# Optimization experiments

Hardware: AMD Instinct MI355X
Metric: run time of the kernel (lower is better)

Reference implementation:

```python
import jax, jax.numpy as jnp
import numpy as np

B, T, D, H, L = 16, 1500, 512, 1024, 20


def setup_inputs() -> dict:
    key = jax.random.key(0)
    ks = jax.random.split(key, 5)
    return {
        "x": jax.random.normal(ks[0], (B, T, D), dtype=jnp.float32),
        "w1": jax.random.normal(ks[1], (D, H), dtype=jnp.float32) * (1.0 / np.sqrt(D)),
        "b1": jax.random.normal(ks[2], (H,), dtype=jnp.float32) * 0.01,
        "wp": jax.random.normal(ks[3], (H, D), dtype=jnp.float32) * (1.0 / np.sqrt(H)),
        "wa": jax.random.normal(ks[4], (D, L), dtype=jnp.float32) * (1.0 / np.sqrt(D)),
    }


def reference(x, w1, b1, wp, wa):
    # x: [B,T,D]
    f1 = jax.nn.relu(x @ w1 + b1)          # [B,T,H]
    p1 = f1 @ wp                            # [B,T,D] (output_dim == input_dim)
    lorder = wa.shape[1]
    t = p1.shape[1]
    # left-pad time axis with lorder-1 zeros so shift i looks at p1[t-i]
    padded = jnp.pad(p1, ((0, 0), (lorder - 1, 0), (0, 0)))  # [B,T+L-1,D]
    # z[..., i] = p1 shifted back by i frames (zero for t-i < 0)
    z = jnp.stack(
        [jax.lax.dynamic_slice_in_dim(padded, lorder - 1 - i, t, axis=1)
         for i in range(lorder)],
        axis=-1,
    )  # [B,T,D,L]
    att = jax.nn.softmax(x @ wa, axis=-1)   # [B,T,L]
    out1 = jnp.einsum('btdl,btl->btd', z, att)
    return x + out1
```

## Files before the change

### kernel.cpp

```cpp
#include <hip/hip_runtime.h>
#include <hip/hip_bf16.h>

#define Bd 16
#define Td 1500
#define Dd 512
#define Hd 1024
#define Ld 20
#define Md (Bd*Td)

using f32x4  = __attribute__((ext_vector_type(4))) float;
using short8 = __attribute__((ext_vector_type(8))) short;

__device__ __forceinline__ unsigned short f2bf(float f) {
    union { float f; unsigned u; } v; v.f = f;
    unsigned r = v.u + 0x7fffu + ((v.u >> 16) & 1u);
    return (unsigned short)(r >> 16);
}
__device__ __forceinline__ float bf2f(unsigned short u) {
    union { unsigned u; float f; } v; v.u = ((unsigned)u) << 16;
    return v.f;
}
__device__ __forceinline__ void gload_lds16(const void* g, void* l) {
    __builtin_amdgcn_global_load_lds(
        (const __attribute__((address_space(1))) unsigned*)g,
        (__attribute__((address_space(3))) unsigned*)l, 16, 0, 0);
}

__device__ __forceinline__ void transpose_body(
    const float* __restrict__ W, unsigned short* __restrict__ WT,
    int K, int N, int n0, int k0, int tid, float (*tile)[33])
{
    const int tx = tid & 31, ty = tid >> 5;
#pragma unroll
    for (int j = 0; j < 32; j += 8)
        tile[ty + j][tx] = W[(size_t)(k0 + ty + j) * N + n0 + tx];
    __syncthreads();
#pragma unroll
    for (int j = 0; j < 32; j += 8)
        WT[(size_t)(n0 + ty + j) * K + k0 + tx] = f2bf(tile[tx][ty + j]);
}

__global__ __launch_bounds__(256) void prep_kernel(
    const float* __restrict__ x,  const float* __restrict__ w1,
    const float* __restrict__ wp, const float* __restrict__ wa,
    unsigned short* __restrict__ xb,  unsigned short* __restrict__ w1T,
    unsigned short* __restrict__ wpT, unsigned short* __restrict__ waT)
{
    __shared__ float tile[32][33];
    const int b = blockIdx.x, tid = threadIdx.x;
    if (b < 6000) {
        size_t i = ((size_t)b * 256 + tid) * 8;
        float4 v0 = *(const float4*)(x + i);
        float4 v1 = *(const float4*)(x + i + 4);
        union { unsigned short us[8]; int4 v; } p;
        p.us[0] = f2bf(v0.x); p.us[1] = f2bf(v0.y); p.us[2] = f2bf(v0.z); p.us[3] = f2bf(v0.w);
        p.us[4] = f2bf(v1.x); p.us[5] = f2bf(v1.y); p.us[6] = f2bf(v1.z); p.us[7] = f2bf(v1.w);
        *(int4*)(xb + i) = p.v;
    } else if (b < 6512) {
        const int idx = b - 6000;
        transpose_body(w1, w1T, Dd, Hd, (idx & 31) * 32, (idx >> 5) * 32, tid, tile);
    } else if (b < 7024) {
        const int idx = b - 6512;
        transpose_body(wp, wpT, Hd, Dd, (idx & 15) * 32, (idx >> 4) * 32, tid, tile);
    } else {
        const int i = (b - 7024) * 256 + tid;
        const int c = i >> 9, d = i & 511;
        waT[i] = (c < Ld) ? f2bf(wa[(size_t)d * Ld + c]) : (unsigned short)0;
    }
}

template<bool RELU_BIAS>
__global__ __launch_bounds__(512) void gemm_lds(
    const unsigned short* __restrict__ A, const unsigned short* __restrict__ BT,
    const float* __restrict__ bias, unsigned short* __restrict__ C,
    int Mdim, int Ndim, int Kdim)
{
    __shared__ __align__(16) unsigned short SH[3 * 8192 + 3 * 4096];

    const int tid  = threadIdx.x;
    const int lane = tid & 63;
    const int wave = tid >> 6;
    const int wr   = wave >> 1, wc = wave & 1;

    const int nx  = gridDim.x;
    const int nwg = nx * gridDim.y;
    const int id  = blockIdx.y * nx + blockIdx.x;
    const int nid = (id & 7) * (nwg >> 3) + (id >> 3);
    const int m0  = (nid / nx) * 256;
    const int n0  = (nid % nx) * 128;

    const int srow  = tid >> 2;
    const int sslot = (tid & 3) ^ ((srow >> 1) & 3);
    int aR0 = m0 + srow;       if (aR0 >= Mdim) aR0 = Mdim - 1;
    int aR1 = m0 + 128 + srow; if (aR1 >= Mdim) aR1 = Mdim - 1;
    const unsigned short* a0p = A  + (size_t)aR0 * Kdim + sslot * 8;
    const unsigned short* a1p = A  + (size_t)aR1 * Kdim + sslot * 8;
    const unsigned short* b0p = BT + (size_t)(n0 + srow) * Kdim + sslot * 8;

    const int rsel = lane & 15;
    const int koff = ((lane >> 4) ^ ((lane >> 1) & 3)) * 8;

    f32x4 acc[4][4] = {};
    const int NT = Kdim >> 5;

    auto stage = [&](int t, int b) {
        const int kk = t * 32;
        gload_lds16(a0p + kk, SH + b * 8192 + wave * 512);
        gload_lds16(a1p + kk, SH + b * 8192 + 4096 + wave * 512);
        gload_lds16(b0p + kk, SH + 24576 + b * 4096 + wave * 512);
    };

    stage(0, 0);
    stage(1, 1);

    int buf = 0;
    for (int t = 0; t < NT; ++t) {
        if (t + 1 < NT) asm volatile("s_waitcnt vmcnt(3)" ::: "memory");
        else            asm volatile("s_waitcnt vmcnt(0)" ::: "memory");
        __builtin_amdgcn_s_barrier();
        asm volatile("" ::: "memory");

        if (t + 2 < NT) {
            int nb = buf + 2; if (nb >= 3) nb -= 3;
            stage(t + 2, nb);
        }

        const unsigned short* as = SH + buf * 8192;
        const unsigned short* bs = SH + 24576 + buf * 4096;
        short8 af[4], bfr[4];
#pragma unroll
        for (int m = 0; m < 4; ++m)
            af[m] = *(const short8*)&as[(wr * 64 + m * 16 + rsel) * 32 + koff];
#pragma unroll
        for (int n = 0; n < 4; ++n)
            bfr[n] = *(const short8*)&bs[(wc * 64 + n * 16 + rsel) * 32 + koff];

        __builtin_amdgcn_s_setprio(1);
#pragma unroll
        for (int m = 0; m < 4; ++m)
#pragma unroll
            for (int n = 0; n < 4; ++n)
                acc[m][n] = __builtin_amdgcn_mfma_f32_16x16x32_bf16(af[m], bfr[n], acc[m][n], 0, 0, 0);
        __builtin_amdgcn_s_setprio(0);

        ++buf; if (buf == 3) buf = 0;
    }

    __syncthreads();
    unsigned short* Cs = SH;

    const int rB = wr * 64 + ((lane >> 4) << 2);
    const int cB = wc * 64;
#pragma unroll
    for (int n = 0; n < 4; ++n) {
        const int col = cB + n * 16 + rsel;
        float bvs = 0.f;
        if (RELU_BIAS) bvs = bias[n0 + col];
        const int s = col >> 3, e = col & 7;
#pragma unroll
        for (int m = 0; m < 4; ++m) {
#pragma unroll
            for (int j = 0; j < 4; ++j) {
                const int r = rB + m * 16 + j;
                float v = acc[m][n][j];
                if (RELU_BIAS) v = fmaxf(v + bvs, 0.f);
                Cs[r * 128 + ((s ^ (r & 7)) << 3) + e] = f2bf(v);
            }
        }
    }
    __syncthreads();

    const int row = tid >> 1;
    const int c0  = (tid & 1) * 64;
    const int gr  = m0 + row;
    if (gr < Mdim) {
#pragma unroll
        for (int i = 0; i < 8; ++i) {
            const int s = (c0 >> 3) + i;
            int4 v = *(const int4*)&Cs[row * 128 + ((s ^ (row & 7)) << 3)];
            *(int4*)&C[(size_t)gr * Ndim + n0 + c0 + i * 8] = v;
        }
    }
}

__global__ __launch_bounds__(256) void att_mfma_kernel(
    const unsigned short* __restrict__ xb, const unsigned short* __restrict__ waT,
    float* __restrict__ att)
{
    __shared__ __align__(16) unsigned short waTs[16 * 1024];
    __shared__ __align__(16) unsigned short As[3][64 * 32];
    __shared__ float sS[64][21];

    const int tid  = threadIdx.x;
    const int lane = tid & 63;
    const int wave = tid >> 6;
    const int m0   = blockIdx.x * 64;

    for (int i = tid; i < 2048; i += 256) {
        const int off = i * 8;
        const int kt = off >> 10, c = (off >> 5) & 31, sl = (off >> 3) & 3;
        const int ssl = sl ^ ((c >> 1) & 3);
        *(short8*)&waTs[off] = *(const short8*)&waT[(size_t)c * Dd + kt * 32 + ssl * 8];
    }
    __syncthreads();

    const int srow  = tid >> 2;
    const int sslot = (tid & 3) ^ ((tid >> 3) & 3);
    const unsigned short* a0p = xb + (size_t)(m0 + srow) * Dd + sslot * 8;

    const int rsel = lane & 15;
    const int koff = ((lane >> 4) ^ ((lane >> 1) & 3)) * 8;

    f32x4 acc[2] = {};

    gload_lds16(a0p, &As[0][wave * 512]);
    gload_lds16(a0p + 32, &As[1][wave * 512]);

    int buf = 0;
    for (int t = 0; t < 16; ++t) {
        if (t < 15) asm volatile("s_waitcnt vmcnt(1)" ::: "memory");
        else        asm volatile("s_waitcnt vmcnt(0)" ::: "memory");
        __builtin_amdgcn_s_barrier();
        asm volatile("" ::: "memory");

        if (t + 2 < 16) {
            int nb = buf + 2; if (nb >= 3) nb -= 3;
            gload_lds16(a0p + (t + 2) * 32, &As[nb][wave * 512]);
        }

        short8 af = *(const short8*)&As[buf][(wave * 16 + rsel) * 32 + koff];
        short8 b0 = *(const short8*)&waTs[t * 1024 + (rsel) * 32 + koff];
        short8 b1 = *(const short8*)&waTs[t * 1024 + (16 + rsel) * 32 + koff];
        acc[0] = __builtin_amdgcn_mfma_f32_16x16x32_bf16(af, b0, acc[0], 0, 0, 0);
        acc[1] = __builtin_amdgcn_mfma_f32_16x16x32_bf16(af, b1, acc[1], 0, 0, 0);

        ++buf; if (buf == 3) buf = 0;
    }

    const int r0 = wave * 16 + ((lane >> 4) << 2);
#pragma unroll
    for (int n = 0; n < 2; ++n) {
        const int c = n * 16 + rsel;
        if (c < 21) {
#pragma unroll
            for (int j = 0; j < 4; ++j)
                sS[r0 + j][c] = acc[n][j];
        }
    }
    __syncthreads();

    if (tid < 64) {
        float mx = -1e30f;
#pragma unroll
        for (int l = 0; l < Ld; ++l) mx = fmaxf(mx, sS[tid][l]);
        float e[Ld]; float sum = 0.f;
#pragma unroll
        for (int l = 0; l < Ld; ++l) { e[l] = __expf(sS[tid][l] - mx); sum += e[l]; }
        const float inv = 1.f / sum;
        const int grow = m0 + tid;
#pragma unroll
        for (int l = 0; l < Ld; ++l)
            att[(size_t)grow * Ld + l] = e[l] * inv;
    }
}

__global__ __launch_bounds__(512) void out_kernel(
    const float* __restrict__ x, const unsigned short* __restrict__ p1,
    const float* __restrict__ att, float* __restrict__ out)
{
    const int bid = blockIdx.x;
    const int nid = (bid & 7) * 375 + (bid >> 3);
    const int wave = threadIdx.x >> 6;
    const int lane = threadIdx.x & 63;
    const int row  = nid * 8 + wave;
    const int t    = row % Td;
    const int d0   = lane * 8;

    float av[Ld];
    const float* ar = att + (size_t)row * Ld;
#pragma unroll
    for (int i = 0; i < Ld; i += 4) {
        float4 v = *(const float4*)(ar + i);
        av[i] = v.x; av[i + 1] = v.y; av[i + 2] = v.z; av[i + 3] = v.w;
    }

    const float* xr = x + (size_t)row * Dd + d0;
    float4 xa = *(const float4*)xr;
    float4 xb4 = *(const float4*)(xr + 4);
    float acc[8] = { xa.x, xa.y, xa.z, xa.w, xb4.x, xb4.y, xb4.z, xb4.w };

    const int imax = (t < Ld - 1) ? t : (Ld - 1);
    const unsigned short* pr = p1 + (size_t)row * Dd + d0;
    for (int i = 0; i <= imax; ++i) {
        const float a = av[i];
        short8 p = *(const short8*)(pr - (size_t)i * Dd);
#pragma unroll
        for (int j = 0; j < 8; ++j) acc[j] += a * bf2f((unsigned short)p[j]);
    }
    float* orow = out + (size_t)row * Dd + d0;
    float4 o0 = { acc[0], acc[1], acc[2], acc[3] };
    float4 o1 = { acc[4], acc[5], acc[6], acc[7] };
    *(float4*)orow       = o0;
    *(float4*)(orow + 4) = o1;
}

extern "C" void kernel_launch(void* const* d_in, const int* in_sizes, int n_in,
                              void* d_out, int out_size, void* d_ws, size_t ws_size,
                              hipStream_t stream)
{
    const float* x  = (const float*)d_in[0];
    const float* w1 = (const float*)d_in[1];
    const float* b1 = (const float*)d_in[2];
    const float* wp = (const float*)d_in[3];
    const float* wa = (const float*)d_in[4];
    float* out = (float*)d_out;

    char* ws = (char*)d_ws;
    unsigned short* xb  = (unsigned short*)ws;  ws += (size_t)Md * Dd * 2;
    unsigned short* w1T = (unsigned short*)ws;  ws += (size_t)Hd * Dd * 2;
    unsigned short* wpT = (unsigned short*)ws;  ws += (size_t)Dd * Hd * 2;
    unsigned short* waT = (unsigned short*)ws;  ws += (size_t)32 * Dd * 2;
    unsigned short* f1  = (unsigned short*)ws;  ws += (size_t)Md * Hd * 2;
    unsigned short* p1  = (unsigned short*)ws;  ws += (size_t)Md * Dd * 2;
    float*          att = (float*)ws;           ws += (size_t)Md * Ld * 4;

    prep_kernel<<<7088, 256, 0, stream>>>(x, w1, wp, wa, xb, w1T, wpT, waT);

    att_mfma_kernel<<<Md / 64, 256, 0, stream>>>(xb, waT, att);

    const int mtiles = (Md + 255) / 256;
    gemm_lds<true ><<<dim3(Hd / 128, mtiles), 512, 0, stream>>>(xb, w1T, b1, f1, Md, Hd, Dd);
    gemm_lds<false><<<dim3(Dd / 128, mtiles), 512, 0, stream>>>(f1, wpT, nullptr, p1, Md, Dd, Hd);

    out_kernel<<<Md / 8, 512, 0, stream>>>(x, p1, att, out);
}
```

Baseline: 216.3 us.

## Halve GEMM waves with larger per-wave tiles; stage p1 window in LDS for output

The GEMM now launches 256 threads (4 waves) per 256x128 tile, so each wave computes a 128x64 sub-tile with 8x4 MFMA accumulators and issues six async global->LDS loads per stage. This raises the register count and the MFMA-to-load ratio per wave. The output kernel now processes 32 consecutive rows per block and loads a 51-row window of p1 into LDS once, so the 20 shifted reads come from shared memory instead of repeated global loads. The risks are lower occupancy from the larger accumulators and heavy LDS use in the output kernel.

Result: slower. 240.2 us (+11.1%).

```diff
diff --git a/kernel.cpp b/kernel.cpp
--- a/kernel.cpp
+++ b/kernel.cpp
@@ -70,12 +70,12 @@
 }
 
 template<bool RELU_BIAS>
-__global__ __launch_bounds__(512) void gemm_lds(
+__global__ __launch_bounds__(256) void gemm_lds(
     const unsigned short* __restrict__ A, const unsigned short* __restrict__ BT,
     const float* __restrict__ bias, unsigned short* __restrict__ C,
     int Mdim, int Ndim, int Kdim)
 {
-    __shared__ __align__(16) unsigned short SH[3 * 8192 + 3 * 4096];
+    __shared__ __align__(16) unsigned short SH[3 * 12288];
 
     const int tid  = threadIdx.x;
     const int lane = tid & 63;
@@ -89,25 +89,35 @@
     const int m0  = (nid / nx) * 256;
     const int n0  = (nid % nx) * 128;
 
-    const int srow  = tid >> 2;
-    const int sslot = (tid & 3) ^ ((srow >> 1) & 3);
-    int aR0 = m0 + srow;       if (aR0 >= Mdim) aR0 = Mdim - 1;
-    int aR1 = m0 + 128 + srow; if (aR1 >= Mdim) aR1 = Mdim - 1;
-    const unsigned short* a0p = A  + (size_t)aR0 * Kdim + sslot * 8;
-    const unsigned short* a1p = A  + (size_t)aR1 * Kdim + sslot * 8;
-    const unsigned short* b0p = BT + (size_t)(n0 + srow) * Kdim + sslot * 8;
+    const int sR    = lane >> 2;
+    const int sslot = (lane & 3) ^ ((lane >> 3) & 3);
+    const unsigned short* aP[4];
+    const unsigned short* bP[2];
+#pragma unroll
+    for (int g = 0; g < 4; ++g) {
+        int r = m0 + g * 64 + wave * 16 + sR;
+        if (r >= Mdim) r = Mdim - 1;
+        aP[g] = A + (size_t)r * Kdim + sslot * 8;
+    }
+#pragma unroll
+    for (int g = 0; g < 2; ++g)
+        bP[g] = BT + (size_t)(n0 + g * 64 + wave * 16 + sR) * Kdim + sslot * 8;
 
     const int rsel = lane & 15;
     const int koff = ((lane >> 4) ^ ((lane >> 1) & 3)) * 8;
 
-    f32x4 acc[4][4] = {};
+    f32x4 acc[8][4] = {};
     const int NT = Kdim >> 5;
 
     auto stage = [&](int t, int b) {
         const int kk = t * 32;
-        gload_lds16(a0p + kk, SH + b * 8192 + wave * 512);
-        gload_lds16(a1p + kk, SH + b * 8192 + 4096 + wave * 512);
-        gload_lds16(b0p + kk, SH + 24576 + b * 4096 + wave * 512);
+        unsigned short* dst = SH + b * 12288;
+#pragma unroll
+        for (int g = 0; g < 4; ++g)
+            gload_lds16(aP[g] + kk, dst + g * 2048 + wave * 512);
+#pragma unroll
+        for (int g = 0; g < 2; ++g)
+            gload_lds16(bP[g] + kk, dst + 8192 + g * 2048 + wave * 512);
     };
 
     stage(0, 0);
@@ -115,7 +125,7 @@
 
     int buf = 0;
     for (int t = 0; t < NT; ++t) {
-        if (t + 1 < NT) asm volatile("s_waitcnt vmcnt(3)" ::: "memory");
+        if (t + 1 < NT) asm volatile("s_waitcnt vmcnt(6)" ::: "memory");
         else            asm volatile("s_waitcnt vmcnt(0)" ::: "memory");
         __builtin_amdgcn_s_barrier();
         asm volatile("" ::: "memory");
@@ -125,19 +135,19 @@
             stage(t + 2, nb);
         }
 
-        const unsigned short* as = SH + buf * 8192;
-        const unsigned short* bs = SH + 24576 + buf * 4096;
-        short8 af[4], bfr[4];
-#pragma unroll
-        for (int m = 0; m < 4; ++m)
-            af[m] = *(const short8*)&as[(wr * 64 + m * 16 + rsel) * 32 + koff];
+        const unsigned short* as = SH + buf * 12288;
+        const unsigned short* bs = as + 8192;
+        short8 bfr[4], af[8];
 #pragma unroll
         for (int n = 0; n < 4; ++n)
             bfr[n] = *(const short8*)&bs[(wc * 64 + n * 16 + rsel) * 32 + koff];
+#pragma unroll
+        for (int m = 0; m < 8; ++m)
+            af[m] = *(const short8*)&as[(wr * 128 + m * 16 + rsel) * 32 + koff];
 
         __builtin_amdgcn_s_setprio(1);
 #pragma unroll
-        for (int m = 0; m < 4; ++m)
+        for (int m = 0; m < 8; ++m)
 #pragma unroll
             for (int n = 0; n < 4; ++n)
                 acc[m][n] = __builtin_amdgcn_mfma_f32_16x16x32_bf16(af[m], bfr[n], acc[m][n], 0, 0, 0);
@@ -149,7 +159,7 @@
     __syncthreads();
     unsigned short* Cs = SH;
 
-    const int rB = wr * 64 + ((lane >> 4) << 2);
+    const int rB = wr * 128 + ((lane >> 4) << 2);
     const int cB = wc * 64;
 #pragma unroll
     for (int n = 0; n < 4; ++n) {
@@ -158,7 +168,7 @@
         if (RELU_BIAS) bvs = bias[n0 + col];
         const int s = col >> 3, e = col & 7;
 #pragma unroll
-        for (int m = 0; m < 4; ++m) {
+        for (int m = 0; m < 8; ++m) {
 #pragma unroll
             for (int j = 0; j < 4; ++j) {
                 const int r = rB + m * 16 + j;
@@ -170,15 +180,13 @@
     }
     __syncthreads();
 
-    const int row = tid >> 1;
-    const int c0  = (tid & 1) * 64;
+    const int row = tid;
     const int gr  = m0 + row;
     if (gr < Mdim) {
 #pragma unroll
-        for (int i = 0; i < 8; ++i) {
-            const int s = (c0 >> 3) + i;
-            int4 v = *(const int4*)&Cs[row * 128 + ((s ^ (row & 7)) << 3)];
-            *(int4*)&C[(size_t)gr * Ndim + n0 + c0 + i * 8] = v;
+        for (int i = 0; i < 16; ++i) {
+            int4 v = *(const int4*)&Cs[row * 128 + ((i ^ (row & 7)) << 3)];
+            *(int4*)&C[(size_t)gr * Ndim + n0 + i * 8] = v;
         }
     }
 }
@@ -268,40 +276,58 @@
     const float* __restrict__ x, const unsigned short* __restrict__ p1,
     const float* __restrict__ att, float* __restrict__ out)
 {
+    __shared__ __align__(16) unsigned short p1w[51 * 512];
+    __shared__ float aS[32 * 20];
+
+    const int tid = threadIdx.x;
     const int bid = blockIdx.x;
-    const int nid = (bid & 7) * 375 + (bid >> 3);
-    const int wave = threadIdx.x >> 6;
-    const int lane = threadIdx.x & 63;
-    const int row  = nid * 8 + wave;
-    const int t    = row % Td;
-    const int d0   = lane * 8;
-
-    float av[Ld];
-    const float* ar = att + (size_t)row * Ld;
-#pragma unroll
-    for (int i = 0; i < Ld; i += 4) {
-        float4 v = *(const float4*)(ar + i);
-        av[i] = v.x; av[i + 1] = v.y; av[i + 2] = v.z; av[i + 3] = v.w;
-    }
-
-    const float* xr = x + (size_t)row * Dd + d0;
-    float4 xa = *(const float4*)xr;
-    float4 xb4 = *(const float4*)(xr + 4);
-    float acc[8] = { xa.x, xa.y, xa.z, xa.w, xb4.x, xb4.y, xb4.z, xb4.w };
-
-    const int imax = (t < Ld - 1) ? t : (Ld - 1);
-    const unsigned short* pr = p1 + (size_t)row * Dd + d0;
+    const int xcd = bid & 7;
+    const int wg  = (xcd < 6 ? xcd * 94 : 564 + (xcd - 6) * 93) + (bid >> 3);
+    const int r0  = wg * 32;
+
+    for (int i = tid; i < 51 * 64; i += 512) {
+        const int rr = i >> 6, cc = i & 63;
+        int gr = r0 - 19 + rr; if (gr < 0) gr = 0;
+        const int pos = (cc >> 2) | ((cc & 3) << 4);
+        *(short8*)&p1w[rr * 512 + pos * 8] = *(const short8*)&p1[(size_t)gr * Dd + cc * 8];
+    }
+    for (int i = tid; i < 32 * Ld; i += 512)
+        aS[i] = att[(size_t)r0 * Ld + i];
+    __syncthreads();
+
+    const int rl  = tid >> 4;
+    const int cl  = tid & 15;
+    const int row = r0 + rl;
+    const int t   = row % Td;
+    const int imax = t < Ld - 1 ? t : Ld - 1;
+
+    float acc[32];
+    const float* xr = x + (size_t)row * Dd + cl * 32;
+#pragma unroll
+    for (int q = 0; q < 8; ++q) {
+        float4 v = *(const float4*)(xr + q * 4);
+        acc[q*4+0] = v.x; acc[q*4+1] = v.y; acc[q*4+2] = v.z; acc[q*4+3] = v.w;
+    }
+
     for (int i = 0; i <= imax; ++i) {
-        const float a = av[i];
-        short8 p = *(const short8*)(pr - (size_t)i * Dd);
-#pragma unroll
-        for (int j = 0; j < 8; ++j) acc[j] += a * bf2f((unsigned short)p[j]);
-    }
-    float* orow = out + (size_t)row * Dd + d0;
-    float4 o0 = { acc[0], acc[1], acc[2], acc[3] };
-    float4 o1 = { acc[4], acc[5], acc[6], acc[7] };
-    *(float4*)orow       = o0;
-    *(float4*)(orow + 4) = o1;
+        const float a = aS[rl * Ld + i];
+        const int R = 19 + rl - i;
+#pragma unroll
+        for (int j = 0; j < 4; ++j) {
+            const int pos = cl | (j << 4);
+            short8 p = *(const short8*)&p1w[R * 512 + pos * 8];
+#pragma unroll
+            for (int e = 0; e < 8; ++e)
+                acc[j*8+e] += a * bf2f((unsigned short)p[e]);
+        }
+    }
+
+    float* orow = out + (size_t)row * Dd + cl * 32;
+#pragma unroll
+    for (int q = 0; q < 8; ++q) {
+        float4 v = { acc[q*4+0], acc[q*4+1], acc[q*4+2], acc[q*4+3] };
+        *(float4*)(orow + q * 4) = v;
+    }
 }
 
 extern "C" void kernel_launch(void* const* d_in, const int* in_sizes, int n_in,
@@ -329,8 +355,8 @@
     att_mfma_kernel<<<Md / 64, 256, 0, stream>>>(xb, waT, att);
 
     const int mtiles = (Md + 255) / 256;
-    gemm_lds<true ><<<dim3(Hd / 128, mtiles), 512, 0, stream>>>(xb, w1T, b1, f1, Md, Hd, Dd);
-    gemm_lds<false><<<dim3(Dd / 128, mtiles), 512, 0, stream>>>(f1, wpT, nullptr, p1, Md, Dd, Hd);
-
-    out_kernel<<<Md / 8, 512, 0, stream>>>(x, p1, att, out);
-}
+    gemm_lds<true ><<<dim3(Hd / 128, mtiles), 256, 0, stream>>>(xb, w1T, b1, f1, Md, Hd, Dd);
+    gemm_lds<false><<<dim3(Dd / 128, mtiles), 256, 0, stream>>>(f1, wpT, nullptr, p1, Md, Dd, Hd);
+
+    out_kernel<<<750, 512, 0, stream>>>(x, p1, att, out);
+}
```

## Use 4-wave GEMM blocks with 128x64 per-wave tiles and double buffering

Applied to the files above, without the earlier changes.

The bf16 GEMM kernel moves from 512 threads (8 waves, 64x64 per wave) to 256 threads (4 waves, each computing a 128x64 sub-tile with 32 accumulators), targeting two blocks per CU. The LDS pipeline changes from triple buffering with two stages in flight to double buffering with one prefetch and two barriers per K-step. The epilogue writes the 256-row tile in two halves through LDS. The aim is more operand reuse per wave and fewer LDS fragment loads per MFMA, at the cost of higher register pressure, shallower prefetch and an extra barrier.

After: 223.3 us. 1.03x slower.

```diff
diff --git a/kernel.cpp b/kernel.cpp
--- a/kernel.cpp
+++ b/kernel.cpp
@@ -70,12 +70,12 @@
 }
 
 template<bool RELU_BIAS>
-__global__ __launch_bounds__(512) void gemm_lds(
+__global__ __launch_bounds__(256, 2) void gemm_lds(
     const unsigned short* __restrict__ A, const unsigned short* __restrict__ BT,
     const float* __restrict__ bias, unsigned short* __restrict__ C,
     int Mdim, int Ndim, int Kdim)
 {
-    __shared__ __align__(16) unsigned short SH[3 * 8192 + 3 * 4096];
+    __shared__ __align__(16) unsigned short SH[2 * 12288];
 
     const int tid  = threadIdx.x;
     const int lane = tid & 63;
@@ -89,97 +89,109 @@
     const int m0  = (nid / nx) * 256;
     const int n0  = (nid % nx) * 128;
 
-    const int srow  = tid >> 2;
-    const int sslot = (tid & 3) ^ ((srow >> 1) & 3);
-    int aR0 = m0 + srow;       if (aR0 >= Mdim) aR0 = Mdim - 1;
-    int aR1 = m0 + 128 + srow; if (aR1 >= Mdim) aR1 = Mdim - 1;
-    const unsigned short* a0p = A  + (size_t)aR0 * Kdim + sslot * 8;
-    const unsigned short* a1p = A  + (size_t)aR1 * Kdim + sslot * 8;
-    const unsigned short* b0p = BT + (size_t)(n0 + srow) * Kdim + sslot * 8;
+    const int sR    = lane >> 2;
+    const int sslot = (lane & 3) ^ ((lane >> 3) & 3);
+    const unsigned short* aP[4];
+    const unsigned short* bP[2];
+#pragma unroll
+    for (int g = 0; g < 4; ++g) {
+        int r = m0 + g * 64 + wave * 16 + sR;
+        if (r >= Mdim) r = Mdim - 1;
+        aP[g] = A + (size_t)r * Kdim + sslot * 8;
+    }
+#pragma unroll
+    for (int g = 0; g < 2; ++g)
+        bP[g] = BT + (size_t)(n0 + g * 64 + wave * 16 + sR) * Kdim + sslot * 8;
 
     const int rsel = lane & 15;
     const int koff = ((lane >> 4) ^ ((lane >> 1) & 3)) * 8;
 
-    f32x4 acc[4][4] = {};
+    f32x4 acc[8][4] = {};
     const int NT = Kdim >> 5;
 
     auto stage = [&](int t, int b) {
         const int kk = t * 32;
-        gload_lds16(a0p + kk, SH + b * 8192 + wave * 512);
-        gload_lds16(a1p + kk, SH + b * 8192 + 4096 + wave * 512);
-        gload_lds16(b0p + kk, SH + 24576 + b * 4096 + wave * 512);
+        unsigned short* dst = SH + b * 12288;
+#pragma unroll
+        for (int g = 0; g < 4; ++g)
+            gload_lds16(aP[g] + kk, dst + g * 2048 + wave * 512);
+#pragma unroll
+        for (int g = 0; g < 2; ++g)
+            gload_lds16(bP[g] + kk, dst + 8192 + g * 2048 + wave * 512);
     };
 
     stage(0, 0);
-    stage(1, 1);
-
-    int buf = 0;
+
     for (int t = 0; t < NT; ++t) {
-        if (t + 1 < NT) asm volatile("s_waitcnt vmcnt(3)" ::: "memory");
-        else            asm volatile("s_waitcnt vmcnt(0)" ::: "memory");
+        const int p = t & 1;
         __builtin_amdgcn_s_barrier();
         asm volatile("" ::: "memory");
-
-        if (t + 2 < NT) {
-            int nb = buf + 2; if (nb >= 3) nb -= 3;
-            stage(t + 2, nb);
-        }
-
-        const unsigned short* as = SH + buf * 8192;
-        const unsigned short* bs = SH + 24576 + buf * 4096;
-        short8 af[4], bfr[4];
-#pragma unroll
-        for (int m = 0; m < 4; ++m)
-            af[m] = *(const short8*)&as[(wr * 64 + m * 16 + rsel) * 32 + koff];
+        if (t + 1 < NT) {
+            stage(t + 1, p ^ 1);
+            asm volatile("s_waitcnt vmcnt(6)" ::: "memory");
+        } else {
+            asm volatile("s_waitcnt vmcnt(0)" ::: "memory");
+        }
+        __builtin_amdgcn_s_barrier();
+        asm volatile("" ::: "memory");
+
+        const unsigned short* as = SH + p * 12288;
+        const unsigned short* bs = as + 8192;
+        short8 bfr[4], af[8];
 #pragma unroll
         for (int n = 0; n < 4; ++n)
             bfr[n] = *(const short8*)&bs[(wc * 64 + n * 16 + rsel) * 32 + koff];
+#pragma unroll
+        for (int m = 0; m < 8; ++m)
+            af[m] = *(const short8*)&as[(wr * 128 + m * 16 + rsel) * 32 + koff];
 
         __builtin_amdgcn_s_setprio(1);
 #pragma unroll
-        for (int m = 0; m < 4; ++m)
+        for (int m = 0; m < 8; ++m)
 #pragma unroll
             for (int n = 0; n < 4; ++n)
                 acc[m][n] = __builtin_amdgcn_mfma_f32_16x16x32_bf16(af[m], bfr[n], acc[m][n], 0, 0, 0);
         __builtin_amdgcn_s_setprio(0);
-
-        ++buf; if (buf == 3) buf = 0;
     }
 
     __syncthreads();
     unsigned short* Cs = SH;
-
-    const int rB = wr * 64 + ((lane >> 4) << 2);
-    const int cB = wc * 64;
-#pragma unroll
-    for (int n = 0; n < 4; ++n) {
-        const int col = cB + n * 16 + rsel;
-        float bvs = 0.f;
-        if (RELU_BIAS) bvs = bias[n0 + col];
-        const int s = col >> 3, e = col & 7;
-#pragma unroll
-        for (int m = 0; m < 4; ++m) {
-#pragma unroll
-            for (int j = 0; j < 4; ++j) {
-                const int r = rB + m * 16 + j;
-                float v = acc[m][n][j];
-                if (RELU_BIAS) v = fmaxf(v + bvs, 0.f);
-                Cs[r * 128 + ((s ^ (r & 7)) << 3) + e] = f2bf(v);
+    const int rloc = (lane >> 4) << 2;
+
+#pragma unroll
+    for (int p = 0; p < 2; ++p) {
+        if (wr == p) {
+#pragma unroll
+            for (int n = 0; n < 4; ++n) {
+                const int col = wc * 64 + n * 16 + rsel;
+                float bvs = 0.f;
+                if (RELU_BIAS) bvs = bias[n0 + col];
+                const int s = col >> 3, e = col & 7;
+#pragma unroll
+                for (int m = 0; m < 8; ++m) {
+#pragma unroll
+                    for (int j = 0; j < 4; ++j) {
+                        const int r = m * 16 + rloc + j;
+                        float v = acc[m][n][j];
+                        if (RELU_BIAS) v = fmaxf(v + bvs, 0.f);
+                        Cs[r * 128 + ((s ^ (r & 7)) << 3) + e] = f2bf(v);
+                    }
+                }
             }
         }
-    }
-    __syncthreads();
-
-    const int row = tid >> 1;
-    const int c0  = (tid & 1) * 64;
-    const int gr  = m0 + row;
-    if (gr < Mdim) {
-#pragma unroll
-        for (int i = 0; i < 8; ++i) {
-            const int s = (c0 >> 3) + i;
-            int4 v = *(const int4*)&Cs[row * 128 + ((s ^ (row & 7)) << 3)];
-            *(int4*)&C[(size_t)gr * Ndim + n0 + c0 + i * 8] = v;
-        }
+        __syncthreads();
+        const int row  = tid >> 1;
+        const int half = tid & 1;
+        const int gr   = m0 + p * 128 + row;
+        if (gr < Mdim) {
+#pragma unroll
+            for (int i = 0; i < 8; ++i) {
+                const int s2 = half * 8 + i;
+                int4 v = *(const int4*)&Cs[row * 128 + ((s2 ^ (row & 7)) << 3)];
+                *(int4*)&C[(size_t)gr * Ndim + n0 + s2 * 8] = v;
+            }
+        }
+        if (p == 0) __syncthreads();
     }
 }
 
@@ -329,8 +341,8 @@
     att_mfma_kernel<<<Md / 64, 256, 0, stream>>>(xb, waT, att);
 
     const int mtiles = (Md + 255) / 256;
-    gemm_lds<true ><<<dim3(Hd / 128, mtiles), 512, 0, stream>>>(xb, w1T, b1, f1, Md, Hd, Dd);
-    gemm_lds<false><<<dim3(Dd / 128, mtiles), 512, 0, stream>>>(f1, wpT, nullptr, p1, Md, Dd, Hd);
+    gemm_lds<true ><<<dim3(Hd / 128, mtiles), 256, 0, stream>>>(xb, w1T, b1, f1, Md, Hd, Dd);
+    gemm_lds<false><<<dim3(Dd / 128, mtiles), 256, 0, stream>>>(f1, wpT, nullptr, p1, Md, Dd, Hd);
 
     out_kernel<<<Md / 8, 512, 0, stream>>>(x, p1, att, out);
 }
```
